# Kernel tuning notes

Measured on AMD Instinct MI355X. Metric: run time of the kernel, lower is better.

## Reference

```python
import jax, jax.numpy as jnp
import numpy as np

B, K, H_IMG, W_IMG = 8, 1, 512, 512
N_ITR = 10      # fixed iteration count (torch max_itr loop, unrolled via scan)
TOL = 1e-3      # convergence tolerance used for per-element gating


def setup_inputs() -> dict:
    key = jax.random.key(0)
    k1, k2 = jax.random.split(key)
    img = jax.random.normal(k1, (B, K, H_IMG, W_IMG), dtype=jnp.float32)
    temp = jax.random.normal(k2, (B, K, H_IMG, W_IMG), dtype=jnp.float32)
    return {"img": img, "temp": temp}


def _grad_batch(F):
    # central difference with replicate padding (== conv with [-0.5,0,0.5])
    px = jnp.pad(F, ((0, 0), (0, 0), (0, 0), (1, 1)), mode='edge')
    dx = 0.5 * (px[..., 2:] - px[..., :-2])
    py = jnp.pad(F, ((0, 0), (0, 0), (1, 1), (0, 0)), mode='edge')
    dy = 0.5 * (py[..., 2:, :] - py[..., :-2, :])
    return dx, dy


def _bilinear_sample(img, xp, yp):
    # img [B,k,h,w]; xp,yp pixel coords [B,h,w]; zeros padding, align_corners=True
    _, k, h, w = img.shape
    x0 = jnp.floor(xp)
    y0 = jnp.floor(yp)
    wx1 = xp - x0
    wy1 = yp - y0

    def tap(xi, yi, wgt):
        valid = (xi >= 0) & (xi <= w - 1) & (yi >= 0) & (yi <= h - 1)
        xc = jnp.clip(xi, 0, w - 1).astype(jnp.int32)
        yc = jnp.clip(yi, 0, h - 1).astype(jnp.int32)
        v = jax.vmap(lambda im, yy, xx: im[:, yy, xx])(img, yc, xc)  # [B,k,h,w]
        return v * (wgt * valid.astype(img.dtype))[:, None]

    return (tap(x0, y0, (1 - wx1) * (1 - wy1)) + tap(x0 + 1, y0, wx1 * (1 - wy1))
            + tap(x0, y0 + 1, (1 - wx1) * wy1) + tap(x0 + 1, y0 + 1, wx1 * wy1))


def _deeplk(img, temp):
    Bb, k, h, w = temp.shape
    gx, gy = _grad_batch(temp)
    # centered pixel coordinates (meshgrid with x - x.max()/2)
    xs = jnp.arange(w, dtype=jnp.float32) - (w - 1) / 2.0
    ys = jnp.arange(h, dtype=jnp.float32) - (h - 1) / 2.0
    X, Y = jnp.meshgrid(xs, ys)  # each [h,w]
    Xf = jnp.tile(X.reshape(-1), k)  # [k*h*w]
    Yf = jnp.tile(Y.reshape(-1), k)
    gxf = gx.reshape(Bb, -1)
    gyf = gy.reshape(Bb, -1)
    # Jacobian dI/dp: [B, k*h*w, 8]
    dIdp = jnp.stack([
        Xf * gxf, Yf * gxf, gxf,
        Xf * gyf, Yf * gyf, gyf,
        -Xf * Xf * gxf - Xf * Yf * gyf,
        -Xf * Yf * gxf - Yf * Yf * gyf], axis=-1)
    Hm = jnp.einsum('bni,bnj->bij', dIdp, dIdp)        # [B,8,8]
    invH = jnp.linalg.inv(Hm)
    invH_dIdp = jnp.einsum('bij,bnj->bin', invH, dIdp)  # [B,8,N]

    xy1 = jnp.stack([X.reshape(-1), Y.reshape(-1),
                     jnp.ones(h * w, jnp.float32)], axis=0)  # [3, h*w]
    I3 = jnp.eye(3, dtype=jnp.float32)

    def param_to_H(p):
        return I3 + jnp.concatenate([p, jnp.zeros((Bb, 1), p.dtype)], 1).reshape(Bb, 3, 3)

    def step(carry, _):
        p, dp = carry  # p,dp: [B,8]
        Hh = param_to_H(p)
        xyw = jnp.einsum('bij,jn->bin', Hh, xy1)
        Xw = (xyw[:, 0] / xyw[:, 2]).reshape(Bb, h, w) + (w - 1) / 2.0
        Yw = (xyw[:, 1] / xyw[:, 2]).reshape(Bb, h, w) + (h - 1) / 2.0
        Fi_warp = _bilinear_sample(img, Xw, Yw)
        xn = Xw / ((w - 1) / 2.0) - 1.0
        yn = Yw / ((h - 1) / 2.0) - 1.0
        mask = ((xn > -1 + 2.0 / w) & (xn < 1 - 2.0 / w) &
                (yn > -1 + 2.0 / h) & (yn < 1 - 2.0 / h)).astype(img.dtype)
        r = (Fi_warp - temp * mask[:, None]).reshape(Bb, -1)  # [B,N]
        dp_new = jnp.einsum('bin,bn->bi', invH_dIdp, r)       # [B,8]
        dp_new = dp_new.at[:, 6:8].set(0.0)                   # no projective update
        gate = (jnp.linalg.norm(dp, axis=1, keepdims=True) > TOL).astype(p.dtype)
        dp_next = gate * dp_new
        return (p - dp_next, dp_next), None

    p0 = jnp.zeros((Bb, 8), jnp.float32)
    dp0 = jnp.ones((Bb, 8), jnp.float32)
    (p, _), _ = jax.lax.scan(step, (p0, dp0), None, length=N_ITR)
    return p.reshape(Bb, 8, 1), param_to_H(p)


def reference(img, temp):
    return _deeplk(img, temp)
```

## Files before the change

kernel.cpp:

```cpp
#include <hip/hip_runtime.h>
#include <math.h>

#define W     512
#define HH    512
#define NB    8
#define NBLK  512
#define TPB   512
#define NW    (TPB / 64)
#define BPB   64
#define ROWS  8
#define NPX   (ROWS * W)
#define PXT   (NPX / TPB)
#define NITR  10
#define POISON64 0xAAAAAAAAAAAAAAAAull
#define ALL64  0xFFFFFFFFFFFFFFFFull

__constant__ const int TJ[36] = {0,0,0,0,0,0,0,0, 1,1,1,1,1,1,1, 2,2,2,2,2,2,
                                 3,3,3,3,3, 4,4,4,4, 5,5,5, 6,6, 7};
__constant__ const int TL[36] = {0,1,2,3,4,5,6,7, 1,2,3,4,5,6,7, 2,3,4,5,6,7,
                                 3,4,5,6,7, 4,5,6,7, 5,6,7, 6,7, 7};

__device__ __forceinline__ float wave_reduce64(float x) {
    x += __shfl_down(x, 32, 64);
    x += __shfl_down(x, 16, 64);
    x += __shfl_down(x, 8, 64);
    x += __shfl_down(x, 4, 64);
    x += __shfl_down(x, 2, 64);
    x += __shfl_down(x, 1, 64);
    return x;
}
__device__ __forceinline__ double load_d(const double* p) {
    unsigned long long u = __hip_atomic_load((const unsigned long long*)p,
                       __ATOMIC_RELAXED, __HIP_MEMORY_SCOPE_AGENT);
    return __builtin_bit_cast(double, u);
}
__device__ __forceinline__ void store_d(double* p, double v) {
    __hip_atomic_store((unsigned long long*)p, __builtin_bit_cast(unsigned long long, v),
                       __ATOMIC_RELAXED, __HIP_MEMORY_SCOPE_AGENT);
}
__device__ __forceinline__ bool not_poison(double v) {
    return __builtin_bit_cast(unsigned long long, v) != POISON64;
}

extern "C" __global__ __launch_bounds__(TPB, 4)
void deeplk_kernel(const float* __restrict__ img, const float* __restrict__ temp,
                   float* __restrict__ out, void* __restrict__ wsv)
{
    double* Hpart = (double*)wsv;
    double* vpart = Hpart + NB * 36 * BPB;

    const int tid   = threadIdx.x;
    const int lane  = tid & 63;
    const int wv    = tid >> 6;
    const int b     = blockIdx.x & 7;
    const int chunk = blockIdx.x >> 3;
    const int row0  = chunk * ROWS;
    const float* tb = temp + b * (HH * W);
    const float* ib = img  + b * (HH * W);

    __shared__ float  s_gx[NPX], s_gy[NPX], s_tv[NPX];
    __shared__ double s_Hu[36];
    __shared__ double s_invH[64];
    __shared__ double s_p[8], s_dp[8], s_v[8];
    __shared__ float  s_wred[NW * 18];
    __shared__ double s_vred[NW * 8];

#pragma unroll
    for (int u = 0; u < PXT; ++u) {
        const int i  = tid + u * TPB;
        const int rr = row0 + (i >> 9);
        const int cc = i & (W - 1);
        const int cl = (cc > 0) ? cc - 1 : 0;
        const int cr = (cc < W - 1) ? cc + 1 : W - 1;
        const int ru = (rr > 0) ? rr - 1 : 0;
        const int rd = (rr < HH - 1) ? rr + 1 : HH - 1;
        s_gx[i] = 0.5f * (tb[rr * W + cr] - tb[rr * W + cl]);
        s_gy[i] = 0.5f * (tb[rd * W + cc] - tb[ru * W + cc]);
        s_tv[i] = tb[rr * W + cc];
    }
    __syncthreads();

#pragma unroll
    for (int grp = 0; grp < 2; ++grp) {
        float acc[18];
#pragma unroll
        for (int k = 0; k < 18; ++k) acc[k] = 0.f;
#pragma unroll
        for (int u = 0; u < PXT; ++u) {
            const int i  = tid + u * TPB;
            const int rr = row0 + (i >> 9);
            const int cc = i & (W - 1);
            const float X = (float)cc - 255.5f;
            const float Y = (float)rr - 255.5f;
            const float gx = s_gx[i], gy = s_gy[i];
            float J[8];
            J[0] = X * gx; J[1] = Y * gx; J[2] = gx;
            J[3] = X * gy; J[4] = Y * gy; J[5] = gy;
            const float sxy = J[0] + J[4];
            J[6] = -X * sxy; J[7] = -Y * sxy;
#pragma unroll
            for (int k = 0; k < 18; ++k)
                acc[k] += J[TJ[grp * 18 + k]] * J[TL[grp * 18 + k]];
        }
#pragma unroll
        for (int k = 0; k < 18; ++k) {
            float x = wave_reduce64(acc[k]);
            if (lane == 0) s_wred[wv * 18 + k] = x;
        }
        __syncthreads();
        if (tid < 18) {
            double s = 0.0;
#pragma unroll
            for (int w2 = 0; w2 < NW; ++w2) s += (double)s_wred[w2 * 18 + tid];
            store_d(&Hpart[(b * 36 + grp * 18 + tid) * BPB + chunk], s);
        }
        __syncthreads();
    }
    for (int c = wv; c < 36; c += NW) {
        const double* hp = &Hpart[(b * 36 + c) * BPB + lane];
        double x;
        for (;;) {
            x = load_d(hp);
            if (__ballot(not_poison(x)) == ALL64) break;
            __builtin_amdgcn_s_sleep(1);
        }
        x += __shfl_down(x, 32, 64);
        x += __shfl_down(x, 16, 64);
        x += __shfl_down(x, 8, 64);
        x += __shfl_down(x, 4, 64);
        x += __shfl_down(x, 2, 64);
        x += __shfl_down(x, 1, 64);
        if (lane == 0) s_Hu[c] = x;
    }
    __syncthreads();

    if (tid < 64) {
        const int r  = tid >> 3, cj = tid & 7;
        const int i2 = (r < cj) ? r : cj;
        const int j2 = (r < cj) ? cj : r;
        double a = s_Hu[i2 * 8 - (i2 * (i2 - 1)) / 2 + (j2 - i2)];
        double e = (r == cj) ? 1.0 : 0.0;
#pragma unroll
        for (int k = 0; k < 8; ++k) {
            int pr = k;
            double pv = fabs(__shfl(a, k * 8 + k, 64));
            for (int rr2 = k + 1; rr2 < 8; ++rr2) {
                double c = fabs(__shfl(a, rr2 * 8 + k, 64));
                if (c > pv) { pv = c; pr = rr2; }
            }
            double a_k = __shfl(a, k * 8 + cj, 64),  e_k = __shfl(e, k * 8 + cj, 64);
            double a_p = __shfl(a, pr * 8 + cj, 64), e_p = __shfl(e, pr * 8 + cj, 64);
            if (r == k)       { a = a_p; e = e_p; }
            else if (r == pr) { a = a_k; e = e_k; }
            double piv = __shfl(a, k * 8 + k, 64);
            double d = 1.0 / piv;
            if (r == k) { a *= d; e *= d; }
            double f  = __shfl(a, r * 8 + k, 64);
            double ak = __shfl(a, k * 8 + cj, 64);
            double ek = __shfl(e, k * 8 + cj, 64);
            if (r != k) { a -= f * ak; e -= f * ek; }
        }
        s_invH[tid] = e;
    }
    if (tid < 8) { s_p[tid] = 0.0; s_dp[tid] = 1.0; }
    __syncthreads();

    for (int it = 0; it < NITR; ++it) {
        double n2 = 0.0;
#pragma unroll
        for (int l = 0; l < 8; ++l) { double d = s_dp[l]; n2 += d * d; }
        if (n2 > 1e-6) {
            const float a00 = 1.f + (float)s_p[0];
            const float a01 = (float)s_p[1];
            const float a02 = (float)s_p[2] + 255.5f;
            const float a10 = (float)s_p[3];
            const float a11 = 1.f + (float)s_p[4];
            const float a12 = (float)s_p[5] + 255.5f;
            float va[8];
#pragma unroll
            for (int c = 0; c < 8; ++c) va[c] = 0.f;

#pragma unroll
            for (int u = 0; u < PXT; ++u) {
                const int i  = tid + u * TPB;
                const int rr = row0 + (i >> 9);
                const int cc = i & (W - 1);
                const float X = (float)cc - 255.5f;
                const float Y = (float)rr - 255.5f;
                const float Xw = a00 * X + a01 * Y + a02;
                const float Yw = a10 * X + a11 * Y + a12;
                const float xf = floorf(Xw), yf = floorf(Yw);
                const int ix = (int)xf, iy = (int)yf;
                const float wx = Xw - xf, wy = Yw - yf;
                const bool vx0 = (ix >= 0) & (ix < W);
                const bool vx1 = (ix >= -1) & (ix < W - 1);
                const bool vy0 = (iy >= 0) & (iy < HH);
                const bool vy1 = (iy >= -1) & (iy < HH - 1);
                const float* ro0 = ib + iy * W;
                const float* ro1 = ro0 + W;
                const float t00 = (vx0 && vy0) ? ro0[ix]     : 0.f;
                const float t10 = (vx1 && vy0) ? ro0[ix + 1] : 0.f;
                const float t01 = (vx0 && vy1) ? ro1[ix]     : 0.f;
                const float t11 = (vx1 && vy1) ? ro1[ix + 1] : 0.f;
                const float Fi = t00 * (1.f - wx) * (1.f - wy) + t10 * wx * (1.f - wy)
                               + t01 * (1.f - wx) * wy + t11 * wx * wy;
                const float xn = Xw * (1.f / 255.5f) - 1.f;
                const float yn = Yw * (1.f / 255.5f) - 1.f;
                const float LO = -1.f + 2.f / 512.f;
                const float HI =  1.f - 2.f / 512.f;
                const float m = (xn > LO && xn < HI && yn > LO && yn < HI) ? 1.f : 0.f;
                const float rv = Fi - s_tv[i] * m;
                const float gx = s_gx[i], gy = s_gy[i];
                const float j0 = X * gx, j1 = Y * gx, j3 = X * gy, j4 = Y * gy;
                const float sxy = j0 + j4;
                va[0] += j0 * rv;  va[1] += j1 * rv;  va[2] += gx * rv;
                va[3] += j3 * rv;  va[4] += j4 * rv;  va[5] += gy * rv;
                va[6] += -X * sxy * rv;  va[7] += -Y * sxy * rv;
            }
#pragma unroll
            for (int c = 0; c < 8; ++c) {
                float x = wave_reduce64(va[c]);
                if (lane == 0) s_wred[wv * 8 + c] = x;
            }
            __syncthreads();
            double* vp = vpart + ((it * NB) + b) * BPB * 8;
            if (tid < 8) {
                double s = 0.0;
#pragma unroll
                for (int w2 = 0; w2 < NW; ++w2) s += (double)s_wred[w2 * 8 + tid];
                store_d(&vp[chunk * 8 + tid], s);
            }
            {
                const double* slot = &vp[tid];
                double x;
                for (;;) {
                    x = load_d(slot);
                    if (__ballot(not_poison(x)) == ALL64) break;
                    __builtin_amdgcn_s_sleep(1);
                }
                x += __shfl_down(x, 32, 64);
                x += __shfl_down(x, 16, 64);
                x += __shfl_down(x, 8, 64);
                if (lane < 8) s_vred[wv * 8 + lane] = x;
            }
            __syncthreads();
            if (tid < 8) {
                double s = 0.0;
#pragma unroll
                for (int w2 = 0; w2 < NW; ++w2) s += s_vred[w2 * 8 + tid];
                s_v[tid] = s;
            }
            __syncthreads();
            if (tid < 8) {
                double dpn = 0.0;
#pragma unroll
                for (int l = 0; l < 8; ++l) dpn += s_invH[tid * 8 + l] * s_v[l];
                if (tid >= 6) dpn = 0.0;
                s_p[tid] -= dpn;
                s_dp[tid] = dpn;
            }
            __syncthreads();
        }
    }

    if (chunk == 0) {
        if (tid < 8) out[b * 8 + tid] = (float)s_p[tid];
        if (tid == 0) {
            float* Ho = out + 64 + b * 9;
            Ho[0] = 1.f + (float)s_p[0]; Ho[1] = (float)s_p[1];       Ho[2] = (float)s_p[2];
            Ho[3] = (float)s_p[3];       Ho[4] = 1.f + (float)s_p[4]; Ho[5] = (float)s_p[5];
            Ho[6] = (float)s_p[6];       Ho[7] = (float)s_p[7];       Ho[8] = 1.f;
        }
    }
}

extern "C" void kernel_launch(void* const* d_in, const int* in_sizes, int n_in,
                              void* d_out, int out_size, void* d_ws, size_t ws_size,
                              hipStream_t stream) {
    const float* img  = (const float*)d_in[0];
    const float* temp = (const float*)d_in[1];
    float* out = (float*)d_out;
    void*  ws  = d_ws;
    void* args[] = { &img, &temp, &out, &ws };
    hipError_t e = hipLaunchCooperativeKernel((const void*)deeplk_kernel, dim3(NBLK),
                                              dim3(TPB), args, 0, stream);
    if (e != hipSuccess) {
        deeplk_kernel<<<dim3(NBLK), dim3(TPB), 0, stream>>>(img, temp, out, ws);
    }
}
```

Measured before the change: 172.5 us.

## Factor Hessian and steepest-descent sums by column to cut per-pixel FLOPs

Each thread now owns one image column, so X is constant per thread. The Hessian is rebuilt from 12 per-column moment sums of gx², gx·gy and gy² weighted by powers of Y, and the per-iteration residual projection accumulates 5 sums in place of 8. The warp coordinates are advanced incrementally across rows, and the mask test is done directly in pixel space. This cuts per-pixel multiply-adds in the Hessian and iteration loops, at the cost of 36 wave reductions computed through a switch and possible float precision loss from higher powers of X and Y.

```diff
diff --git a/kernel.cpp b/kernel.cpp
--- a/kernel.cpp
+++ b/kernel.cpp
@@ -14,11 +14,8 @@
 #define NITR  10
 #define POISON64 0xAAAAAAAAAAAAAAAAull
 #define ALL64  0xFFFFFFFFFFFFFFFFull
-
-__constant__ const int TJ[36] = {0,0,0,0,0,0,0,0, 1,1,1,1,1,1,1, 2,2,2,2,2,2,
-                                 3,3,3,3,3, 4,4,4,4, 5,5,5, 6,6, 7};
-__constant__ const int TL[36] = {0,1,2,3,4,5,6,7, 1,2,3,4,5,6,7, 2,3,4,5,6,7,
-                                 3,4,5,6,7, 4,5,6,7, 5,6,7, 6,7, 7};
+#define MLO 0.998046875f
+#define MHI 510.001953125f
 
 __device__ __forceinline__ float wave_reduce64(float x) {
     x += __shfl_down(x, 32, 64);
@@ -42,6 +39,41 @@
     return __builtin_bit_cast(unsigned long long, v) != POISON64;
 }
 
+__device__ __forceinline__ float hrec(int t, float X1, float X2, float X3, float X4,
+    float a0, float a1, float a2, float b0, float b1, float b2, float b3,
+    float c0, float c1, float c2, float c3, float c4)
+{
+    switch (t) {
+    case 0:  return X2 * a0;             case 1:  return X1 * a1;
+    case 2:  return X1 * a0;             case 3:  return X2 * b0;
+    case 4:  return X1 * b1;             case 5:  return X1 * b0;
+    case 6:  return -(X3 * a0 + X2 * b1);
+    case 7:  return -(X2 * a1 + X1 * b2);
+    case 8:  return a2;                  case 9:  return a1;
+    case 10: return X1 * b1;             case 11: return b2;
+    case 12: return b1;
+    case 13: return -(X2 * a1 + X1 * b2);
+    case 14: return -(X1 * a2 + b3);
+    case 15: return a0;                  case 16: return X1 * b0;
+    case 17: return b1;                  case 18: return b0;
+    case 19: return -(X2 * a0 + X1 * b1);
+    case 20: return -(X1 * a1 + b2);
+    case 21: return X2 * c0;             case 22: return X1 * c1;
+    case 23: return X1 * c0;
+    case 24: return -(X3 * b0 + X2 * c1);
+    case 25: return -(X2 * b1 + X1 * c2);
+    case 26: return c2;                  case 27: return c1;
+    case 28: return -(X2 * b1 + X1 * c2);
+    case 29: return -(X1 * b2 + c3);
+    case 30: return c0;
+    case 31: return -(X2 * b0 + X1 * c1);
+    case 32: return -(X1 * b1 + c2);
+    case 33: return X4 * a0 + 2.f * X3 * b1 + X2 * c2;
+    case 34: return X3 * a1 + 2.f * X2 * b2 + X1 * c3;
+    default: return X2 * a2 + 2.f * X1 * b3 + c4;
+    }
+}
+
 extern "C" __global__ __launch_bounds__(TPB, 4)
 void deeplk_kernel(const float* __restrict__ img, const float* __restrict__ temp,
                    float* __restrict__ out, void* __restrict__ wsv)
@@ -62,14 +94,16 @@
     __shared__ double s_Hu[36];
     __shared__ double s_invH[64];
     __shared__ double s_p[8], s_dp[8], s_v[8];
-    __shared__ float  s_wred[NW * 18];
+    __shared__ float  s_wred[NW * 9];
     __shared__ double s_vred[NW * 8];
+
+    const float X1 = (float)tid - 255.5f;
 
 #pragma unroll
     for (int u = 0; u < PXT; ++u) {
         const int i  = tid + u * TPB;
-        const int rr = row0 + (i >> 9);
-        const int cc = i & (W - 1);
+        const int rr = row0 + u;
+        const int cc = tid;
         const int cl = (cc > 0) ? cc - 1 : 0;
         const int cr = (cc < W - 1) ? cc + 1 : W - 1;
         const int ru = (rr > 0) ? rr - 1 : 0;
@@ -80,41 +114,43 @@
     }
     __syncthreads();
 
-#pragma unroll
-    for (int grp = 0; grp < 2; ++grp) {
-        float acc[18];
-#pragma unroll
-        for (int k = 0; k < 18; ++k) acc[k] = 0.f;
+    float a0 = 0.f, a1 = 0.f, a2 = 0.f;
+    float b0 = 0.f, b1 = 0.f, b2 = 0.f, b3 = 0.f;
+    float c0 = 0.f, c1 = 0.f, c2 = 0.f, c3 = 0.f, c4 = 0.f;
+    {
+        float Yv = (float)row0 - 255.5f;
 #pragma unroll
         for (int u = 0; u < PXT; ++u) {
-            const int i  = tid + u * TPB;
-            const int rr = row0 + (i >> 9);
-            const int cc = i & (W - 1);
-            const float X = (float)cc - 255.5f;
-            const float Y = (float)rr - 255.5f;
+            const int i = tid + u * TPB;
             const float gx = s_gx[i], gy = s_gy[i];
-            float J[8];
-            J[0] = X * gx; J[1] = Y * gx; J[2] = gx;
-            J[3] = X * gy; J[4] = Y * gy; J[5] = gy;
-            const float sxy = J[0] + J[4];
-            J[6] = -X * sxy; J[7] = -Y * sxy;
-#pragma unroll
-            for (int k = 0; k < 18; ++k)
-                acc[k] += J[TJ[grp * 18 + k]] * J[TL[grp * 18 + k]];
-        }
-#pragma unroll
-        for (int k = 0; k < 18; ++k) {
-            float x = wave_reduce64(acc[k]);
-            if (lane == 0) s_wred[wv * 18 + k] = x;
-        }
-        __syncthreads();
-        if (tid < 18) {
-            double s = 0.0;
-#pragma unroll
-            for (int w2 = 0; w2 < NW; ++w2) s += (double)s_wred[w2 * 18 + tid];
-            store_d(&Hpart[(b * 36 + grp * 18 + tid) * BPB + chunk], s);
-        }
-        __syncthreads();
+            const float q1 = gx * gx, q2 = gx * gy, q3 = gy * gy;
+            const float y2 = Yv * Yv, y3 = y2 * Yv, y4 = y2 * y2;
+            a0 += q1; a1 += Yv * q1; a2 += y2 * q1;
+            b0 += q2; b1 += Yv * q2; b2 += y2 * q2; b3 += y3 * q2;
+            c0 += q3; c1 += Yv * q3; c2 += y2 * q3; c3 += y3 * q3; c4 += y4 * q3;
+            Yv += 1.f;
+        }
+    }
+    {
+        const float X2 = X1 * X1, X3 = X2 * X1, X4 = X2 * X2;
+#pragma unroll
+        for (int grp = 0; grp < 4; ++grp) {
+#pragma unroll
+            for (int k = 0; k < 9; ++k) {
+                float x = wave_reduce64(hrec(grp * 9 + k, X1, X2, X3, X4,
+                                             a0, a1, a2, b0, b1, b2, b3,
+                                             c0, c1, c2, c3, c4));
+                if (lane == 0) s_wred[wv * 9 + k] = x;
+            }
+            __syncthreads();
+            if (tid < 9) {
+                double s = 0.0;
+#pragma unroll
+                for (int w2 = 0; w2 < NW; ++w2) s += (double)s_wred[w2 * 9 + tid];
+                store_d(&Hpart[(b * 36 + grp * 9 + tid) * BPB + chunk], s);
+            }
+            __syncthreads();
+        }
     }
     for (int c = wv; c < 36; c += NW) {
         const double* hp = &Hpart[(b * 36 + c) * BPB + lane];
@@ -176,19 +212,14 @@
             const float a10 = (float)s_p[3];
             const float a11 = 1.f + (float)s_p[4];
             const float a12 = (float)s_p[5] + 255.5f;
-            float va[8];
-#pragma unroll
-            for (int c = 0; c < 8; ++c) va[c] = 0.f;
+            float Yv = (float)row0 - 255.5f;
+            float Xw = a00 * X1 + a01 * Yv + a02;
+            float Yw = a10 * X1 + a11 * Yv + a12;
+            float A = 0.f, Bv = 0.f, Cv = 0.f, Dv = 0.f, Ev = 0.f;
 
 #pragma unroll
             for (int u = 0; u < PXT; ++u) {
-                const int i  = tid + u * TPB;
-                const int rr = row0 + (i >> 9);
-                const int cc = i & (W - 1);
-                const float X = (float)cc - 255.5f;
-                const float Y = (float)rr - 255.5f;
-                const float Xw = a00 * X + a01 * Y + a02;
-                const float Yw = a10 * X + a11 * Y + a12;
+                const int i = tid + u * TPB;
                 const float xf = floorf(Xw), yf = floorf(Yw);
                 const int ix = (int)xf, iy = (int)yf;
                 const float wx = Xw - xf, wy = Yw - yf;
@@ -202,20 +233,24 @@
                 const float t10 = (vx1 && vy0) ? ro0[ix + 1] : 0.f;
                 const float t01 = (vx0 && vy1) ? ro1[ix]     : 0.f;
                 const float t11 = (vx1 && vy1) ? ro1[ix + 1] : 0.f;
-                const float Fi = t00 * (1.f - wx) * (1.f - wy) + t10 * wx * (1.f - wy)
-                               + t01 * (1.f - wx) * wy + t11 * wx * wy;
-                const float xn = Xw * (1.f / 255.5f) - 1.f;
-                const float yn = Yw * (1.f / 255.5f) - 1.f;
-                const float LO = -1.f + 2.f / 512.f;
-                const float HI =  1.f - 2.f / 512.f;
-                const float m = (xn > LO && xn < HI && yn > LO && yn < HI) ? 1.f : 0.f;
+                const float omx = 1.f - wx, omy = 1.f - wy;
+                const float Fi = (t00 * omx + t10 * wx) * omy
+                               + (t01 * omx + t11 * wx) * wy;
+                const float m = (Xw > MLO && Xw < MHI && Yw > MLO && Yw < MHI) ? 1.f : 0.f;
                 const float rv = Fi - s_tv[i] * m;
-                const float gx = s_gx[i], gy = s_gy[i];
-                const float j0 = X * gx, j1 = Y * gx, j3 = X * gy, j4 = Y * gy;
-                const float sxy = j0 + j4;
-                va[0] += j0 * rv;  va[1] += j1 * rv;  va[2] += gx * rv;
-                va[3] += j3 * rv;  va[4] += j4 * rv;  va[5] += gy * rv;
-                va[6] += -X * sxy * rv;  va[7] += -Y * sxy * rv;
+                const float t1 = s_gx[i] * rv, t2 = s_gy[i] * rv;
+                A  += t1;        Bv += t2;
+                Cv += Yv * t1;   Dv += Yv * t2;
+                Ev += (Yv * Yv) * t2;
+                Xw += a01; Yw += a11; Yv += 1.f;
+            }
+            float va[8];
+            {
+                const float X2 = X1 * X1;
+                va[0] = X1 * A;  va[1] = Cv;  va[2] = A;
+                va[3] = X1 * Bv; va[4] = Dv;  va[5] = Bv;
+                va[6] = -(X2 * A + X1 * Dv);
+                va[7] = -(X1 * Cv + Ev);
             }
 #pragma unroll
             for (int c = 0; c < 8; ++c) {
```

New measurement: 164.7 us. 4.6% less time.
